# Kernel optimization log

Measured on AMD Instinct MI355X. Metric: run time of the kernel, lower is better.

The kernel has to match this reference:

```python
import jax, jax.numpy as jnp
import numpy as np

N = 50000      # nodes
E = 1_600_000  # edges
DIN, HID, OUT, H = 128, 32, 32, 4


def _glorot(key, shape):
    fan_in, fan_out = shape[0], shape[1] if len(shape) > 1 else shape[0]
    s = jnp.sqrt(6.0 / (fan_in + fan_out)).astype(jnp.float32)
    return jax.random.uniform(key, shape, jnp.float32, -s, s)


def setup_inputs() -> dict:
    key = jax.random.key(0)
    ks = jax.random.split(key, 16)
    inp = {
        "x": jax.random.normal(ks[0], (N, DIN), jnp.float32),
        "edge_index": jax.random.randint(ks[1], (2, E), 0, N, dtype=jnp.int32),
        "edge_weight": jax.random.uniform(ks[2], (E, 1), jnp.float32),
        # layer 1: in=DIN, heads=H, out=HID, concat=True
        "Wl1": _glorot(ks[3], (DIN, H * HID)),
        "Wr1": _glorot(ks[4], (DIN, H * HID)),
        "We1": _glorot(ks[5], (1, H * HID)),
        "att1": _glorot(ks[6], (H, HID)),
        "b1": jnp.zeros((H * HID,), jnp.float32),
        # layer 2: in=H*HID, heads=H, out=OUT, concat=False (mean over heads)
        "Wl2": _glorot(ks[7], (H * HID, H * OUT)),
        "Wr2": _glorot(ks[8], (H * HID, H * OUT)),
        "We2": _glorot(ks[9], (1, H * OUT)),
        "att2": _glorot(ks[10], (H, OUT)),
        "b2": jnp.zeros((OUT,), jnp.float32),
    }
    return inp


def gatv2_layer(x, edge_index, edge_weight, Wl, Wr, We, att, b, concat):
    """Faithful PyG GATv2Conv (share_weights=False, negative_slope=0.2,
    add_self_loops=True with fill_value='mean' for edge_attr)."""
    n = x.shape[0]
    heads, c = att.shape
    src, dst = edge_index[0], edge_index[1]
    # add self loops with mean edge weight (PyG default when edge_dim is set)
    loop = jnp.arange(n, dtype=edge_index.dtype)
    src = jnp.concatenate([src, loop])
    dst = jnp.concatenate([dst, loop])
    ew = jnp.concatenate(
        [edge_weight, jnp.full((n, edge_weight.shape[1]), jnp.mean(edge_weight), edge_weight.dtype)], axis=0)

    xl = (x @ Wl).reshape(n, heads, c)   # source transform (lin_l)
    xr = (x @ Wr).reshape(n, heads, c)   # target transform (lin_r)
    e_feat = (ew @ We).reshape(-1, heads, c)

    z = jax.nn.leaky_relu(xl[src] + xr[dst] + e_feat, 0.2)   # [E', H, C]
    logits = jnp.einsum('ehc,hc->eh', z, att)                # [E', H]

    # segment softmax over incoming edges of each target node
    m = jax.ops.segment_max(logits, dst, num_segments=n)
    m = jnp.where(jnp.isfinite(m), m, 0.0)
    p = jnp.exp(logits - m[dst])
    denom = jax.ops.segment_sum(p, dst, num_segments=n)
    alpha = p / (denom[dst] + 1e-16)                          # [E', H]

    out = jax.ops.segment_sum(xl[src] * alpha[..., None], dst, num_segments=n)  # [N, H, C]
    out = out.reshape(n, heads * c) if concat else out.mean(axis=1)
    return out + b


def reference(x, edge_index, edge_weight, Wl1, Wr1, We1, att1, b1,
              Wl2, Wr2, We2, att2, b2):
    h = gatv2_layer(x, edge_index, edge_weight, Wl1, Wr1, We1, att1, b1, concat=True)
    h = jax.nn.elu(h)
    out = gatv2_layer(h, edge_index, edge_weight, Wl2, Wr2, We2, att2, b2, concat=False)
    return out
```

## Files before the change

### kernel.cpp

```cpp
#include <hip/hip_runtime.h>
#include <hip/hip_fp16.h>
#include <math.h>
#include <type_traits>


typedef _Float16 half8 __attribute__((ext_vector_type(8)));
typedef float floatx4 __attribute__((ext_vector_type(4)));

__global__ __launch_bounds__(256) void bucket_hist_sum(
    const int* __restrict__ dst, const float* __restrict__ ew,
    int* __restrict__ bcnt, float* __restrict__ sumbuf, int E) {
    __shared__ int h[256];
    h[threadIdx.x] = 0;
    __syncthreads();
    float s = 0.f;
    for (int i = blockIdx.x * blockDim.x + threadIdx.x; i < E; i += gridDim.x * blockDim.x) {
        atomicAdd(&h[dst[i] >> 8], 1);
        s += ew[i];
    }
#pragma unroll
    for (int off = 1; off <= 32; off <<= 1)
        s += __shfl_xor(s, off, 64);
    if ((threadIdx.x & 63) == 0)
        atomicAdd(sumbuf, s);
    __syncthreads();
    int v = h[threadIdx.x];
    if (v) atomicAdd(&bcnt[threadIdx.x], v);
}

__global__ __launch_bounds__(256) void partition_kernel(
    const int* __restrict__ src, const int* __restrict__ dst, const float* __restrict__ ew,
    const int* __restrict__ bcnt, int* __restrict__ bcur, int* __restrict__ bbase,
    int2* __restrict__ srec, int E, int NBK) {
    __shared__ int ex[256];
    __shared__ int h[256];
    __shared__ int gb[256];
    const int t = threadIdx.x;

    int v = (t < NBK) ? bcnt[t] : 0;
    ex[t] = v;
    __syncthreads();
    for (int off = 1; off < 256; off <<= 1) {
        int y = 0;
        if (t >= off) y = ex[t - off];
        __syncthreads();
        ex[t] += y;
        __syncthreads();
    }
    const int exbase = ex[t] - v;
    if (blockIdx.x == 0 && t <= NBK) bbase[t] = exbase;

    h[t] = 0;
    __syncthreads();
    const int base = blockIdx.x * 2048;
    int d[8], sv[8];
    float wv[8];
#pragma unroll
    for (int j = 0; j < 8; j++) {
        int i = base + t + j * 256;
        if (i < E) {
            d[j] = dst[i];
            sv[j] = src[i];
            wv[j] = ew[i];
            atomicAdd(&h[d[j] >> 8], 1);
        } else {
            d[j] = -1;
        }
    }
    __syncthreads();
    int cntt = h[t];
    if (cntt) gb[t] = exbase + atomicAdd(&bcur[t], cntt);
    h[t] = 0;
    __syncthreads();
#pragma unroll
    for (int j = 0; j < 8; j++) {
        if (d[j] >= 0) {
            int b = d[j] >> 8;
            int r = atomicAdd(&h[b], 1);
            int pos = gb[b] + r;
            srec[pos] = make_int2(sv[j] | ((d[j] & 255) << 20), __float_as_int(wv[j]));
        }
    }
}

__global__ __launch_bounds__(1024) void dst_hist_kernel(
    const int2* __restrict__ srec, const int* __restrict__ bbase,
    int* __restrict__ cnt, int N) {
    __shared__ int h4[4][256];
    const int t = threadIdx.x;
    const int grp = t >> 8, sub = t & 255;
    h4[grp][sub] = 0;
    __syncthreads();
    const int b = blockIdx.x;
    const int e0 = bbase[b], e1 = bbase[b + 1];
    for (int i = e0 + t; i < e1; i += 1024)
        atomicAdd(&h4[grp][(srec[i].x >> 20) & 255], 1);
    __syncthreads();
    if (t < 256) {
        int node = (b << 8) + t;
        if (node < N) cnt[node] = h4[0][t] + h4[1][t] + h4[2][t] + h4[3][t];
    }
}

__global__ void scan1_kernel(const int* __restrict__ cnt, int* __restrict__ rowp,
                             int* __restrict__ bsum, int N) {
    __shared__ int sh[256];
    int i = blockIdx.x * 256 + threadIdx.x;
    int v = (i < N) ? (cnt[i] + 1) : 0;
    sh[threadIdx.x] = v;
    __syncthreads();
    for (int off = 1; off < 256; off <<= 1) {
        int y = 0;
        if ((int)threadIdx.x >= off) y = sh[threadIdx.x - off];
        __syncthreads();
        sh[threadIdx.x] += y;
        __syncthreads();
    }
    int incl = sh[threadIdx.x];
    if (i < N) rowp[i] = incl - v;
    if (threadIdx.x == 255) bsum[blockIdx.x] = incl;
}

__global__ void scan3_kernel(int* __restrict__ rowp, const int* __restrict__ bsum,
                             const int* __restrict__ cnt, const float* __restrict__ sumbuf,
                             int2* __restrict__ crec, int N, int E, int nb) {
    __shared__ int sh[256];
    const int t = threadIdx.x;
    int v = (t < nb) ? bsum[t] : 0;
    sh[t] = v;
    __syncthreads();
    for (int off = 1; off < 256; off <<= 1) {
        int y = 0;
        if (t >= off) y = sh[t - off];
        __syncthreads();
        sh[t] += y;
        __syncthreads();
    }
    int boff = sh[blockIdx.x] - bsum[blockIdx.x];
    int i = blockIdx.x * 256 + t;
    if (i < N) {
        int rp = rowp[i] + boff;
        rowp[i] = rp;
        crec[rp + cnt[i]] = make_int2(i, __float_as_int(sumbuf[0] * (1.0f / (float)E)));
    }
    if (i == 0) rowp[N] = E + N;
}

__global__ __launch_bounds__(1024) void refine_kernel(
    const int2* __restrict__ srec, const int* __restrict__ bbase,
    const int* __restrict__ rowp, int2* __restrict__ crec, int N) {
    __shared__ int cur[256];
    const int t = threadIdx.x;
    const int b = blockIdx.x;
    if (t < 256) {
        int node = (b << 8) + t;
        cur[t] = (node < N) ? rowp[node] : 0;
    }
    __syncthreads();
    const int e0 = bbase[b], e1 = bbase[b + 1];
    for (int i = e0 + t; i < e1; i += 1024) {
        int2 rec = srec[i];
        int dlow = (rec.x >> 20) & 255;
        int pos = atomicAdd(&cur[dlow], 1);
        crec[pos] = make_int2(rec.x & 0xFFFFF, rec.y);
    }
}

__global__ __launch_bounds__(256) void prep_w2_kernel(
    const float* __restrict__ Wa1, const float* __restrict__ Wb1,
    const float* __restrict__ Wa2, const float* __restrict__ Wb2,
    _Float16* __restrict__ Wh1, _Float16* __restrict__ Wh2,
    int* __restrict__ bcnt, int* __restrict__ bcur) {
    const int bid = blockIdx.x;
    if (bid == 0 && threadIdx.x < 260) bcnt[threadIdx.x] = 0;
    if (bid == 1 && threadIdx.x < 260) bcur[threadIdx.x] = 0;
    const int sel = bid >> 7;
    const float* Wa = sel ? Wa2 : Wa1;
    const float* Wb = sel ? Wb2 : Wb1;
    _Float16* Wh = sel ? Wh2 : Wh1;
    int tid = (bid & 127) * 256 + threadIdx.x;
    int j = tid & 7;
    int lane = (tid >> 3) & 63;
    int f = tid >> 9;
    int kk = f & 3;
    int ct = f >> 2;
    int col = ct * 16 + (lane & 15);
    int k = kk * 32 + ((lane >> 4) << 3) + j;
    float v = (col < 128) ? Wa[k * 128 + col] : Wb[k * 128 + (col - 128)];
    Wh[tid] = (_Float16)v;
}

template <typename T>
__global__ __launch_bounds__(256) void gemm_mfma_kernel(
    const T* __restrict__ X, const _Float16* __restrict__ Wh,
    __half* __restrict__ Yh, float* __restrict__ Yb, int N) {
    __shared__ _Float16 Xs[64 * 128];
    const int tid = threadIdx.x;
    const int lane = tid & 63;
    const int w = tid >> 6;
    const int rb = blockIdx.x * 64;

    half8 wf[4][4];
#pragma unroll
    for (int ct = 0; ct < 4; ct++)
#pragma unroll
        for (int kk = 0; kk < 4; kk++)
            wf[ct][kk] = *(const half8*)(Wh + (size_t)(((w * 4 + ct) * 4 + kk) * 512 + lane * 8));

    if constexpr (std::is_same<T, float>::value) {
#pragma unroll
        for (int it = 0; it < 8; it++) {
            int c = it * 256 + tid;
            int row = c >> 5;
            int f4 = c & 31;
            float4 v = make_float4(0.f, 0.f, 0.f, 0.f);
            if (rb + row < N)
                v = ((const float4*)X)[(size_t)(rb + row) * 32 + f4];
            _Float16 h[4] = {(_Float16)v.x, (_Float16)v.y, (_Float16)v.z, (_Float16)v.w};
            int byteoff = row * 256 + ((f4 * 8) ^ ((row & 7) << 4));
            *(uint2*)((char*)Xs + byteoff) = *(uint2*)h;
        }
    } else {
#pragma unroll
        for (int it = 0; it < 4; it++) {
            int c = it * 256 + tid;
            int row = c >> 4;
            int f16 = c & 15;
            int4 v = make_int4(0, 0, 0, 0);
            if (rb + row < N)
                v = ((const int4*)X)[(size_t)(rb + row) * 16 + f16];
            int byteoff = row * 256 + ((f16 * 16) ^ ((row & 7) << 4));
            *(int4*)((char*)Xs + byteoff) = v;
        }
    }
    __syncthreads();

    floatx4 acc[4][4];
#pragma unroll
    for (int ct = 0; ct < 4; ct++)
#pragma unroll
        for (int rt = 0; rt < 4; rt++)
            acc[ct][rt] = (floatx4){0.f, 0.f, 0.f, 0.f};

#pragma unroll
    for (int kk = 0; kk < 4; kk++) {
        half8 xf[4];
#pragma unroll
        for (int rt = 0; rt < 4; rt++) {
            int row = rt * 16 + (lane & 15);
            int kb = kk * 64 + ((lane >> 4) << 4);
            int off = row * 256 + (kb ^ ((row & 7) << 4));
            xf[rt] = *(const half8*)((const char*)Xs + off);
        }
#pragma unroll
        for (int ct = 0; ct < 4; ct++)
#pragma unroll
            for (int rt = 0; rt < 4; rt++)
                acc[ct][rt] = __builtin_amdgcn_mfma_f32_16x16x32_f16(
                    wf[ct][kk], xf[rt], acc[ct][rt], 0, 0, 0);
    }

    const int rsub = lane & 15;
    const int c4 = (lane >> 4) << 2;
#pragma unroll
    for (int ct = 0; ct < 4; ct++) {
        int gct = w * 4 + ct;
#pragma unroll
        for (int rt = 0; rt < 4; rt++) {
            int row = rb + rt * 16 + rsub;
            if (row < N) {
                floatx4 a = acc[ct][rt];
                if (gct < 8) {
                    int col = gct * 16 + c4;
                    __half2 hp[2];
                    hp[0] = __floats2half2_rn(a[0], a[1]);
                    hp[1] = __floats2half2_rn(a[2], a[3]);
                    *(uint2*)(Yh + (size_t)row * 128 + col) = *(uint2*)hp;
                } else {
                    int col = (gct - 8) * 16 + c4;
                    *(float4*)(Yb + (size_t)row * 128 + col) =
                        make_float4(a[0], a[1], a[2], a[3]);
                }
            }
        }
    }
}

template <int CTRL>
__device__ __forceinline__ float dpp_sum_step(float v) {
    int t = __builtin_amdgcn_update_dpp(0, __float_as_int(v), CTRL, 0xF, 0xF, true);
    return v + __int_as_float(t);
}

__device__ __forceinline__ float2 cvt_h2(unsigned u) {
    __half2 h = *(__half2*)&u;
    return __half22float2(h);
}

__global__ __launch_bounds__(256) void agg_kernel(
    const __half* __restrict__ xlh, const float* __restrict__ xr,
    const int* __restrict__ rowp, const int2* __restrict__ crec,
    const float* __restrict__ We, const float* __restrict__ att, const float* __restrict__ bias,
    void* __restrict__ out, int N, int mode) {
    const int wid = threadIdx.x >> 6;
    const int lane = threadIdx.x & 63;
    const int n = blockIdx.x * 4 + wid;
    if (n >= N) return;
    const int g = lane >> 4;
    const int q = lane & 15;
    const int c0 = q << 3;
    const float LOG2E = 1.4426950408889634f;

    float we[8], xv[8], at6[8], at4[8];
    {
        float4 wA = *(const float4*)(We + c0);
        float4 wB = *(const float4*)(We + c0 + 4);
        we[0]=wA.x; we[1]=wA.y; we[2]=wA.z; we[3]=wA.w;
        we[4]=wB.x; we[5]=wB.y; we[6]=wB.z; we[7]=wB.w;
        float4 rA = *(const float4*)(xr + (size_t)n * 128 + c0);
        float4 rB = *(const float4*)(xr + (size_t)n * 128 + c0 + 4);
        xv[0]=rA.x; xv[1]=rA.y; xv[2]=rA.z; xv[3]=rA.w;
        xv[4]=rB.x; xv[5]=rB.y; xv[6]=rB.z; xv[7]=rB.w;
        float4 aA = *(const float4*)(att + c0);
        float4 aB = *(const float4*)(att + c0 + 4);
        float av[8] = {aA.x, aA.y, aA.z, aA.w, aB.x, aB.y, aB.z, aB.w};
#pragma unroll
        for (int c = 0; c < 8; c++) {
            at6[c] = 0.6f * LOG2E * av[c];
            at4[c] = 0.4f * LOG2E * av[c];
        }
    }

    float acc[8];
#pragma unroll
    for (int c = 0; c < 8; c++) acc[c] = 0.f;
    float l0 = 0.f;

    const int e0 = __builtin_amdgcn_readfirstlane(rowp[n]);
    const int e1 = __builtin_amdgcn_readfirstlane(rowp[n + 1]);
    const int cnt = e1 - e0;
    const int T = (cnt + 3) >> 2;

    auto recload = [&](int i) -> int2 {
        int idx = e0 + (i << 2) + g;
        idx = (idx < e1 - 1) ? idx : (e1 - 1);
        return crec[idx];
    };
    auto gatherx = [&](int s) -> int4 {
        return *(const int4*)(xlh + (size_t)s * 128 + c0);
    };
    auto process = [&](int4 xh, float w, bool valid) {
        float2 x01 = cvt_h2(xh.x), x23 = cvt_h2(xh.y);
        float2 x45 = cvt_h2(xh.z), x67 = cvt_h2(xh.w);
        float xs[8] = {x01.x, x01.y, x23.x, x23.y, x45.x, x45.y, x67.x, x67.y};
        float p = 0.f;
#pragma unroll
        for (int c = 0; c < 8; c++) {
            float z = xs[c] + fmaf(w, we[c], xv[c]);
            p = fmaf(at6[c], z, fmaf(at4[c], fabsf(z), p));
        }
        p = dpp_sum_step<0xB1>(p);
        p = dpp_sum_step<0x4E>(p);
        float qe = valid ? __builtin_amdgcn_exp2f(p) : 0.f;
        l0 += qe;
#pragma unroll
        for (int c = 0; c < 8; c++) acc[c] = fmaf(qe, xs[c], acc[c]);
    };

    int2 r0 = recload(0), r1 = recload(1), r2 = recload(2), r3 = recload(3);
    int4 x0 = gatherx(r0.x), x1 = gatherx(r1.x);
    for (int i = 0; i < T; ++i) {
        int2 r4 = recload(i + 4);
        int4 x2 = gatherx(r2.x);
        process(x0, __int_as_float(r0.y), (e0 + (i << 2) + g) < e1);
        r0 = r1; r1 = r2; r2 = r3; r3 = r4;
        x0 = x1; x1 = x2;
    }

    l0 += __shfl_xor(l0, 16, 64);
    l0 += __shfl_xor(l0, 32, 64);
#pragma unroll
    for (int c = 0; c < 8; c++) {
        acc[c] += __shfl_xor(acc[c], 16, 64);
        acc[c] += __shfl_xor(acc[c], 32, 64);
    }
    float rdenom = 1.0f / (l0 + 1e-16f);
    float r[8];
#pragma unroll
    for (int c = 0; c < 8; c++) r[c] = acc[c] * rdenom;

    if (mode == 0) {
        if (g == 0) {
            float4 bA = *(const float4*)(bias + c0);
            float4 bB = *(const float4*)(bias + c0 + 4);
            float bv[8] = {bA.x, bA.y, bA.z, bA.w, bB.x, bB.y, bB.z, bB.w};
            float o[8];
#pragma unroll
            for (int c = 0; c < 8; c++) {
                float v = r[c] + bv[c];
                o[c] = (v > 0.f) ? v : (__expf(v) - 1.f);
            }
            __half2 p0 = __floats2half2_rn(o[0], o[1]);
            __half2 p1 = __floats2half2_rn(o[2], o[3]);
            __half2 p2 = __floats2half2_rn(o[4], o[5]);
            __half2 p3 = __floats2half2_rn(o[6], o[7]);
            int4 pk = make_int4(*(int*)&p0, *(int*)&p1, *(int*)&p2, *(int*)&p3);
            *(int4*)((__half*)out + (size_t)n * 128 + c0) = pk;
        }
    } else {
#pragma unroll
        for (int c = 0; c < 8; c++) {
            r[c] += __shfl_xor(r[c], 4, 64);
            r[c] += __shfl_xor(r[c], 8, 64);
        }
        if (lane < 4) {
            int w0 = lane << 3;
            float4 bA = *(const float4*)(bias + w0);
            float4 bB = *(const float4*)(bias + w0 + 4);
            float bv[8] = {bA.x, bA.y, bA.z, bA.w, bB.x, bB.y, bB.z, bB.w};
            float o[8];
#pragma unroll
            for (int c = 0; c < 8; c++) o[c] = 0.25f * r[c] + bv[c];
            float* op = (float*)out + (size_t)n * 32 + w0;
            *(float4*)op       = make_float4(o[0], o[1], o[2], o[3]);
            *(float4*)(op + 4) = make_float4(o[4], o[5], o[6], o[7]);
        }
    }
}

extern "C" void kernel_launch(void* const* d_in, const int* in_sizes, int n_in,
                              void* d_out, int out_size, void* d_ws, size_t ws_size,
                              hipStream_t stream) {
    const float* x    = (const float*)d_in[0];
    const int*  eidx  = (const int*)d_in[1];
    const float* ew   = (const float*)d_in[2];
    const float* Wl1  = (const float*)d_in[3];
    const float* Wr1  = (const float*)d_in[4];
    const float* We1  = (const float*)d_in[5];
    const float* att1 = (const float*)d_in[6];
    const float* b1   = (const float*)d_in[7];
    const float* Wl2  = (const float*)d_in[8];
    const float* Wr2  = (const float*)d_in[9];
    const float* We2  = (const float*)d_in[10];
    const float* att2 = (const float*)d_in[11];
    const float* b2   = (const float*)d_in[12];

    const int N = in_sizes[0] / 128;
    const int E = in_sizes[1] / 2;
    const int* src = eidx;
    const int* dst = eidx + E;
    const int NBK = (N + 255) >> 8;

    char* p = (char*)d_ws;
    auto alloc = [&](size_t bytes) -> void* {
        void* r = (void*)p;
        p += (bytes + 255) & ~(size_t)255;
        return r;
    };
    __half* xlh   = (__half*)alloc((size_t)N * 128 * sizeof(__half));
    float* xr     = (float*)alloc((size_t)N * 128 * sizeof(float));
    __half* h1h   = (__half*)alloc((size_t)N * 128 * sizeof(float));
    int2*  crec   = (int2*)alloc((size_t)(E + N + 64) * sizeof(int2));
    int*   rowp   = (int*)alloc((size_t)(N + 1) * sizeof(int));
    int*   cnt    = (int*)alloc((size_t)N * sizeof(int));
    int*   bcnt   = (int*)alloc(260 * sizeof(int));
    float* sumbuf = (float*)(bcnt + 256);
    int*   bbase  = (int*)alloc(260 * sizeof(int));
    int*   bcur   = (int*)alloc(260 * sizeof(int));
    int*   bsum   = (int*)alloc(256 * sizeof(int));
    _Float16* Wh1 = (_Float16*)alloc(32768 * sizeof(_Float16));
    _Float16* Wh2 = (_Float16*)alloc(32768 * sizeof(_Float16));
    int2*  srec   = (int2*)h1h;

    prep_w2_kernel<<<256, 256, 0, stream>>>(Wl1, Wr1, Wl2, Wr2, Wh1, Wh2,
                                            bcnt, bcur);

    bucket_hist_sum<<<1024, 256, 0, stream>>>(dst, ew, bcnt, sumbuf, E);
    partition_kernel<<<(E + 2047) / 2048, 256, 0, stream>>>(
        src, dst, ew, bcnt, bcur, bbase, srec, E, NBK);
    dst_hist_kernel<<<NBK, 1024, 0, stream>>>(srec, bbase, cnt, N);

    int nb = (N + 255) / 256;
    scan1_kernel<<<nb, 256, 0, stream>>>(cnt, rowp, bsum, N);
    scan3_kernel<<<nb, 256, 0, stream>>>(rowp, bsum, cnt, sumbuf, crec, N, E, nb);

    refine_kernel<<<NBK, 1024, 0, stream>>>(srec, bbase, rowp, crec, N);

    gemm_mfma_kernel<float><<<(N + 63) / 64, 256, 0, stream>>>(x, Wh1, xlh, xr, N);
    agg_kernel<<<(N + 3) / 4, 256, 0, stream>>>(xlh, xr, rowp, crec,
                                                We1, att1, b1, (void*)h1h, N, 0);
    gemm_mfma_kernel<_Float16><<<(N + 63) / 64, 256, 0, stream>>>(
        (const _Float16*)h1h, Wh2, xlh, xr, N);
    agg_kernel<<<(N + 3) / 4, 256, 0, stream>>>(xlh, xr, rowp, crec,
                                                We2, att2, b2, d_out, N, 1);
}
```

Before: 363.1 us.

## Fuse dst histogram, scans and refine into one per-bucket CSR build kernel

Replaces four kernels (dst histogram, two-level scan, refine) with a single per-bucket kernel. It derives each bucket's global row offset from the already-known bucket base plus the bucket's node index, and does the scan locally in shared memory. This removes three launches and the global cnt/bsum round trips during CSR construction. It relies on bucket bases being exact edge prefix sums so that row pointers stay consistent across buckets.

Result: faster. 354.0 us (-2.5%).

```diff
diff --git a/kernel.cpp b/kernel.cpp
--- a/kernel.cpp
+++ b/kernel.cpp
@@ -83,10 +83,13 @@
     }
 }
 
-__global__ __launch_bounds__(1024) void dst_hist_kernel(
+__global__ __launch_bounds__(1024) void build_csr_kernel(
     const int2* __restrict__ srec, const int* __restrict__ bbase,
-    int* __restrict__ cnt, int N) {
+    const float* __restrict__ sumbuf, int* __restrict__ rowp,
+    int2* __restrict__ crec, int N, int E) {
     __shared__ int h4[4][256];
+    __shared__ int sc[256];
+    __shared__ int cur[256];
     const int t = threadIdx.x;
     const int grp = t >> 8, sub = t & 255;
     h4[grp][sub] = 0;
@@ -96,68 +99,32 @@
     for (int i = e0 + t; i < e1; i += 1024)
         atomicAdd(&h4[grp][(srec[i].x >> 20) & 255], 1);
     __syncthreads();
+    int deg = 0;
+    if (t < 256) {
+        deg = h4[0][t] + h4[1][t] + h4[2][t] + h4[3][t];
+        int node = (b << 8) + t;
+        sc[t] = (node < N) ? (deg + 1) : 0;
+    }
+    __syncthreads();
+    for (int off = 1; off < 256; off <<= 1) {
+        int y = 0;
+        if (t < 256 && t >= off) y = sc[t - off];
+        __syncthreads();
+        if (t < 256) sc[t] += y;
+        __syncthreads();
+    }
+    const int base = bbase[b] + (b << 8);
     if (t < 256) {
         int node = (b << 8) + t;
-        if (node < N) cnt[node] = h4[0][t] + h4[1][t] + h4[2][t] + h4[3][t];
-    }
-}
-
-__global__ void scan1_kernel(const int* __restrict__ cnt, int* __restrict__ rowp,
-                             int* __restrict__ bsum, int N) {
-    __shared__ int sh[256];
-    int i = blockIdx.x * 256 + threadIdx.x;
-    int v = (i < N) ? (cnt[i] + 1) : 0;
-    sh[threadIdx.x] = v;
-    __syncthreads();
-    for (int off = 1; off < 256; off <<= 1) {
-        int y = 0;
-        if ((int)threadIdx.x >= off) y = sh[threadIdx.x - off];
-        __syncthreads();
-        sh[threadIdx.x] += y;
-        __syncthreads();
-    }
-    int incl = sh[threadIdx.x];
-    if (i < N) rowp[i] = incl - v;
-    if (threadIdx.x == 255) bsum[blockIdx.x] = incl;
-}
-
-__global__ void scan3_kernel(int* __restrict__ rowp, const int* __restrict__ bsum,
-                             const int* __restrict__ cnt, const float* __restrict__ sumbuf,
-                             int2* __restrict__ crec, int N, int E, int nb) {
-    __shared__ int sh[256];
-    const int t = threadIdx.x;
-    int v = (t < nb) ? bsum[t] : 0;
-    sh[t] = v;
-    __syncthreads();
-    for (int off = 1; off < 256; off <<= 1) {
-        int y = 0;
-        if (t >= off) y = sh[t - off];
-        __syncthreads();
-        sh[t] += y;
-        __syncthreads();
-    }
-    int boff = sh[blockIdx.x] - bsum[blockIdx.x];
-    int i = blockIdx.x * 256 + t;
-    if (i < N) {
-        int rp = rowp[i] + boff;
-        rowp[i] = rp;
-        crec[rp + cnt[i]] = make_int2(i, __float_as_int(sumbuf[0] * (1.0f / (float)E)));
-    }
-    if (i == 0) rowp[N] = E + N;
-}
-
-__global__ __launch_bounds__(1024) void refine_kernel(
-    const int2* __restrict__ srec, const int* __restrict__ bbase,
-    const int* __restrict__ rowp, int2* __restrict__ crec, int N) {
-    __shared__ int cur[256];
-    const int t = threadIdx.x;
-    const int b = blockIdx.x;
-    if (t < 256) {
-        int node = (b << 8) + t;
-        cur[t] = (node < N) ? rowp[node] : 0;
-    }
-    __syncthreads();
-    const int e0 = bbase[b], e1 = bbase[b + 1];
+        if (node < N) {
+            int rp = base + sc[t] - (deg + 1);
+            rowp[node] = rp;
+            cur[t] = rp;
+            crec[rp + deg] = make_int2(node, __float_as_int(sumbuf[0] * (1.0f / (float)E)));
+            if (node == N - 1) rowp[N] = E + N;
+        }
+    }
+    __syncthreads();
     for (int i = e0 + t; i < e1; i += 1024) {
         int2 rec = srec[i];
         int dlow = (rec.x >> 20) & 255;
@@ -462,12 +429,10 @@
     __half* h1h   = (__half*)alloc((size_t)N * 128 * sizeof(float));
     int2*  crec   = (int2*)alloc((size_t)(E + N + 64) * sizeof(int2));
     int*   rowp   = (int*)alloc((size_t)(N + 1) * sizeof(int));
-    int*   cnt    = (int*)alloc((size_t)N * sizeof(int));
     int*   bcnt   = (int*)alloc(260 * sizeof(int));
     float* sumbuf = (float*)(bcnt + 256);
     int*   bbase  = (int*)alloc(260 * sizeof(int));
     int*   bcur   = (int*)alloc(260 * sizeof(int));
-    int*   bsum   = (int*)alloc(256 * sizeof(int));
     _Float16* Wh1 = (_Float16*)alloc(32768 * sizeof(_Float16));
     _Float16* Wh2 = (_Float16*)alloc(32768 * sizeof(_Float16));
     int2*  srec   = (int2*)h1h;
@@ -478,13 +443,8 @@
     bucket_hist_sum<<<1024, 256, 0, stream>>>(dst, ew, bcnt, sumbuf, E);
     partition_kernel<<<(E + 2047) / 2048, 256, 0, stream>>>(
         src, dst, ew, bcnt, bcur, bbase, srec, E, NBK);
-    dst_hist_kernel<<<NBK, 1024, 0, stream>>>(srec, bbase, cnt, N);
-
-    int nb = (N + 255) / 256;
-    scan1_kernel<<<nb, 256, 0, stream>>>(cnt, rowp, bsum, N);
-    scan3_kernel<<<nb, 256, 0, stream>>>(rowp, bsum, cnt, sumbuf, crec, N, E, nb);
-
-    refine_kernel<<<NBK, 1024, 0, stream>>>(srec, bbase, rowp, crec, N);
+    build_csr_kernel<<<NBK, 1024, 0, stream>>>(srec, bbase, sumbuf, rowp,
+                                               crec, N, E);
 
     gemm_mfma_kernel<float><<<(N + 63) / 64, 256, 0, stream>>>(x, Wh1, xlh, xr, N);
     agg_kernel<<<(N + 3) / 4, 256, 0, stream>>>(xlh, xr, rowp, crec,
```
